# Kernel tuning notes

Measured on AMD Instinct MI355X. Metric: run time of the kernel, lower is better.

## Reference

```python
import jax, jax.numpy as jnp
import numpy as np

CAPACITY_FACTOR_EVAL = 2.0
MIN_CAPACITY = 4


def setup_inputs() -> dict:
    key = jax.random.key(0)
    inputs = jax.random.normal(key, (8192, 64), dtype=jnp.float32)
    return {"inputs": inputs}


def _get_capacity(s, e):
    cap = int(np.floor(CAPACITY_FACTOR_EVAL * s / e))
    cap += cap % 2
    return max(cap, MIN_CAPACITY)


def reference(inputs):
    # inputs: [s, e] router logits
    s, e = inputs.shape
    capacity = _get_capacity(s, e)  # static python int

    # autocast softmax in fp32
    logits = jax.nn.softmax(inputs.astype(jnp.float32), axis=-1)  # [s, e]

    top1_idx = jnp.argmax(logits, axis=-1)                         # [s]
    mask1 = jax.nn.one_hot(top1_idx, e, dtype=jnp.int32)           # [s, e]
    logits_except1 = jnp.where(mask1.astype(bool), -jnp.inf, logits)
    top2_idx = jnp.argmax(logits_except1, axis=-1)                 # [s]
    mask2 = jax.nn.one_hot(top2_idx, e, dtype=jnp.int32)           # [s, e]

    # moe_cumsum: exclusive position rank per expert (cumsum - 1)
    rank1 = jnp.cumsum(mask1, axis=0) - 1                          # [s, e]
    rank2 = jnp.cumsum(mask2, axis=0) - 1
    rank2 = rank2 + jnp.sum(mask1, axis=0, keepdims=True)          # offset by top1 counts

    # drop tokens beyond capacity
    mask1 = mask1 * (rank1 < capacity).astype(jnp.int32)
    mask2 = mask2 * (rank2 < capacity).astype(jnp.int32)

    rank1 = jnp.sum(mask1 * rank1, axis=-1)                        # [s]
    rank2 = jnp.sum(mask2 * rank2, axis=-1)                        # [s]

    weight1 = mask1.astype(logits.dtype) * logits                  # [s, e]
    weight2 = mask2.astype(logits.dtype) * logits

    rank1_sc = jax.nn.one_hot(rank1, capacity, dtype=logits.dtype) # [s, c]
    rank2_sc = jax.nn.one_hot(rank2, capacity, dtype=logits.dtype)

    # combine weights: [s, e, c]
    cb_weight = weight1[:, :, None] * rank1_sc[:, None, :] + weight2[:, :, None] * rank2_sc[:, None, :]
    sec_mask = cb_weight != 0
    return cb_weight, sec_mask
```

## Files before the change

kernel.cpp:

```cpp
#include <hip/hip_runtime.h>
#include <math.h>

#define S 8192
#define E 64
#define CAP 256
static const long long NOUT = (long long)S * E * CAP;
static const long long NQ   = (2 * NOUT) / 4;

typedef float f32x4 __attribute__((ext_vector_type(4)));

__global__ void softmax_top2(const float* __restrict__ in,
                             int* __restrict__ idx1, int* __restrict__ idx2,
                             float* __restrict__ w1, float* __restrict__ w2) {
    const int lane = threadIdx.x;
    const int row  = blockIdx.x * 4 + threadIdx.y;

    float x = in[row * E + lane];

    float mx = x;
    #pragma unroll
    for (int o = 32; o > 0; o >>= 1) mx = fmaxf(mx, __shfl_xor(mx, o));

    float p = __expf(x - mx);
    float sum = p;
    #pragma unroll
    for (int o = 32; o > 0; o >>= 1) sum += __shfl_xor(sum, o);
    float prob = p / sum;

    float v = x; int idx = lane;
    #pragma unroll
    for (int o = 32; o > 0; o >>= 1) {
        float ov = __shfl_xor(v, o);
        int   oi = __shfl_xor(idx, o);
        if (ov > v || (ov == v && oi < idx)) { v = ov; idx = oi; }
    }
    const int i1 = idx;

    float x2 = (lane == i1) ? -INFINITY : x;
    v = x2; idx = lane;
    #pragma unroll
    for (int o = 32; o > 0; o >>= 1) {
        float ov = __shfl_xor(v, o);
        int   oi = __shfl_xor(idx, o);
        if (ov > v || (ov == v && oi < idx)) { v = ov; idx = oi; }
    }
    const int i2 = idx;

    const float pw1 = __shfl(prob, i1);
    const float pw2 = __shfl(prob, i2);

    if (lane == 0) {
        idx1[row] = i1;
        idx2[row] = i2;
        w1[row]   = pw1;
        w2[row]   = pw2;
    }
}

__global__ __launch_bounds__(256) void fill_zero(f32x4* __restrict__ out) {
    const size_t i = (size_t)blockIdx.x * 256 + threadIdx.x;
    const f32x4 z = {0.f, 0.f, 0.f, 0.f};
    out[i] = z;
}

__global__ __launch_bounds__(256) void rank_scatter(
        const int* __restrict__ idx1, const int* __restrict__ idx2,
        const float* __restrict__ w1, const float* __restrict__ w2,
        float* __restrict__ out) {
    const int e    = blockIdx.x;
    const int lane = threadIdx.x & 63;
    const int w    = threadIdx.x >> 6;
    const int seg  = S / 4;
    const int t0w  = w * seg;
    const unsigned long long below = (1ULL << lane) - 1ULL;

    __shared__ int c1s[4], c2s[4];

    int c1 = 0, c2 = 0;
    #pragma unroll 4
    for (int t0 = t0w; t0 < t0w + seg; t0 += 64) {
        const int t = t0 + lane;
        c1 += __popcll(__ballot(idx1[t] == e));
        c2 += __popcll(__ballot(idx2[t] == e));
    }
    if (lane == 0) { c1s[w] = c1; c2s[w] = c2; }
    __syncthreads();

    const int tot1 = c1s[0] + c1s[1] + c1s[2] + c1s[3];
    int off1 = 0, off2 = tot1;
    for (int k = 0; k < w; ++k) { off1 += c1s[k]; off2 += c2s[k]; }

    int base = off1;
    #pragma unroll 4
    for (int t0 = t0w; t0 < t0w + seg; t0 += 64) {
        const int t = t0 + lane;
        const int iv = idx1[t];
        const unsigned long long m = __ballot(iv == e);
        if (iv == e) {
            const int r = base + __popcll(m & below);
            if (r < CAP) {
                const float v = w1[t];
                const long long off = (long long)t * (E * CAP) + e * CAP + r;
                out[off]        = v;
                out[NOUT + off] = (v != 0.0f) ? 1.0f : 0.0f;
            }
        }
        base += __popcll(m);
    }
    base = off2;
    #pragma unroll 4
    for (int t0 = t0w; t0 < t0w + seg; t0 += 64) {
        const int t = t0 + lane;
        const int iv = idx2[t];
        const unsigned long long m = __ballot(iv == e);
        if (iv == e) {
            const int r = base + __popcll(m & below);
            if (r < CAP) {
                const float v = w2[t];
                const long long off = (long long)t * (E * CAP) + e * CAP + r;
                out[off]        = v;
                out[NOUT + off] = (v != 0.0f) ? 1.0f : 0.0f;
            }
        }
        base += __popcll(m);
    }
}

extern "C" void kernel_launch(void* const* d_in, const int* in_sizes, int n_in,
                              void* d_out, int out_size, void* d_ws, size_t ws_size,
                              hipStream_t stream) {
    const float* in = (const float*)d_in[0];
    float* out = (float*)d_out;

    int*   idx1 = (int*)d_ws;
    int*   idx2 = idx1 + S;
    float* w1   = (float*)(idx2 + S);
    float* w2   = w1 + S;

    softmax_top2<<<S / 4, dim3(64, 4), 0, stream>>>(in, idx1, idx2, w1, w2);
    fill_zero<<<(int)(NQ / 256), 256, 0, stream>>>((f32x4*)out);
    rank_scatter<<<E, 256, 0, stream>>>(idx1, idx2, w1, w2, out);
}
```

Baseline: 201.6 us.

## Fuse zero-fill and scatter into one dense output pass driven by per-token table

Rank computation now writes a compact per-token table holding the flat slot index and weight for top-1 and top-2. A single dense fill kernel then produces each output vector, with zeros except at the matching slots. This drops the separate zero-fill and the scattered writes that followed it, so the large output is written only once. In exchange, every output thread reads a table entry and does a few compares.

```diff
diff --git a/kernel.cpp b/kernel.cpp
--- a/kernel.cpp
+++ b/kernel.cpp
@@ -5,13 +5,14 @@
 #define E 64
 #define CAP 256
 static const long long NOUT = (long long)S * E * CAP;
-static const long long NQ   = (2 * NOUT) / 4;
+static const long long NQH  = NOUT / 4;
 
 typedef float f32x4 __attribute__((ext_vector_type(4)));
+typedef int   i32x4 __attribute__((ext_vector_type(4)));
 
 __global__ void softmax_top2(const float* __restrict__ in,
                              int* __restrict__ idx1, int* __restrict__ idx2,
-                             float* __restrict__ w1, float* __restrict__ w2) {
+                             i32x4* __restrict__ table) {
     const int lane = threadIdx.x;
     const int row  = blockIdx.x * 4 + threadIdx.y;
 
@@ -52,21 +53,15 @@
     if (lane == 0) {
         idx1[row] = i1;
         idx2[row] = i2;
-        w1[row]   = pw1;
-        w2[row]   = pw2;
+        int* tp = (int*)&table[row];
+        tp[1] = __float_as_int(pw1);
+        tp[3] = __float_as_int(pw2);
     }
 }
 
-__global__ __launch_bounds__(256) void fill_zero(f32x4* __restrict__ out) {
-    const size_t i = (size_t)blockIdx.x * 256 + threadIdx.x;
-    const f32x4 z = {0.f, 0.f, 0.f, 0.f};
-    out[i] = z;
-}
-
-__global__ __launch_bounds__(256) void rank_scatter(
+__global__ __launch_bounds__(256) void rank_pack(
         const int* __restrict__ idx1, const int* __restrict__ idx2,
-        const float* __restrict__ w1, const float* __restrict__ w2,
-        float* __restrict__ out) {
+        i32x4* __restrict__ table) {
     const int e    = blockIdx.x;
     const int lane = threadIdx.x & 63;
     const int w    = threadIdx.x >> 6;
@@ -94,16 +89,10 @@
     #pragma unroll 4
     for (int t0 = t0w; t0 < t0w + seg; t0 += 64) {
         const int t = t0 + lane;
-        const int iv = idx1[t];
-        const unsigned long long m = __ballot(iv == e);
-        if (iv == e) {
+        const unsigned long long m = __ballot(idx1[t] == e);
+        if (idx1[t] == e) {
             const int r = base + __popcll(m & below);
-            if (r < CAP) {
-                const float v = w1[t];
-                const long long off = (long long)t * (E * CAP) + e * CAP + r;
-                out[off]        = v;
-                out[NOUT + off] = (v != 0.0f) ? 1.0f : 0.0f;
-            }
+            ((int*)&table[t])[0] = (r < CAP) ? (e * CAP + r) : -1;
         }
         base += __popcll(m);
     }
@@ -111,19 +100,38 @@
     #pragma unroll 4
     for (int t0 = t0w; t0 < t0w + seg; t0 += 64) {
         const int t = t0 + lane;
-        const int iv = idx2[t];
-        const unsigned long long m = __ballot(iv == e);
-        if (iv == e) {
+        const unsigned long long m = __ballot(idx2[t] == e);
+        if (idx2[t] == e) {
             const int r = base + __popcll(m & below);
-            if (r < CAP) {
-                const float v = w2[t];
-                const long long off = (long long)t * (E * CAP) + e * CAP + r;
-                out[off]        = v;
-                out[NOUT + off] = (v != 0.0f) ? 1.0f : 0.0f;
-            }
+            ((int*)&table[t])[2] = (r < CAP) ? (e * CAP + r) : -1;
         }
         base += __popcll(m);
     }
+}
+
+__global__ __launch_bounds__(256) void fill_patch(
+        const i32x4* __restrict__ table, f32x4* __restrict__ out) {
+    const long long i = (long long)blockIdx.x * 256 + threadIdx.x;
+    const bool mask_half = (i >= NQH);
+    const long long j = mask_half ? i - NQH : i;
+    const int t  = (int)(j >> 12);
+    const int rq = ((int)j & 4095) << 2;
+    const i32x4 te = table[t];
+
+    float v1 = __int_as_float(te.y);
+    float v2 = __int_as_float(te.w);
+    if (mask_half) {
+        v1 = (v1 != 0.0f) ? 1.0f : 0.0f;
+        v2 = (v2 != 0.0f) ? 1.0f : 0.0f;
+    }
+
+    f32x4 v = {0.f, 0.f, 0.f, 0.f};
+    #pragma unroll
+    for (int k = 0; k < 4; ++k) {
+        if (te.x == rq + k) v[k] = v1;
+        if (te.z == rq + k) v[k] = v2;
+    }
+    out[i] = v;
 }
 
 extern "C" void kernel_launch(void* const* d_in, const int* in_sizes, int n_in,
@@ -132,12 +140,11 @@
     const float* in = (const float*)d_in[0];
     float* out = (float*)d_out;
 
-    int*   idx1 = (int*)d_ws;
-    int*   idx2 = idx1 + S;
-    float* w1   = (float*)(idx2 + S);
-    float* w2   = w1 + S;
+    int*   idx1  = (int*)d_ws;
+    int*   idx2  = idx1 + S;
+    i32x4* table = (i32x4*)(idx2 + S);
 
-    softmax_top2<<<S / 4, dim3(64, 4), 0, stream>>>(in, idx1, idx2, w1, w2);
-    fill_zero<<<(int)(NQ / 256), 256, 0, stream>>>((f32x4*)out);
-    rank_scatter<<<E, 256, 0, stream>>>(idx1, idx2, w1, w2, out);
+    softmax_top2<<<S / 4, dim3(64, 4), 0, stream>>>(in, idx1, idx2, table);
+    rank_pack<<<E, 256, 0, stream>>>(idx1, idx2, table);
+    fill_patch<<<(int)(2 * NQH / 256), 256, 0, stream>>>(table, (f32x4*)out);
 }
```

After: 231.4 us. 14.8% more time.
